# Performance work log

Hardware: AMD Instinct MI355X
Metric: run time of the kernel (lower is better)

The kernel has to match this reference:

```python
import jax, jax.numpy as jnp
import numpy as np

NUM_BLOCKS = 2
RES_LAYERS = 10
HID = 128
IN_CH = 256
MID_CH = 512
OUT_CH = 256
DILATIONS = [2 ** l for b in range(NUM_BLOCKS) for l in range(RES_LAYERS)]
GOOD = sum(DILATIONS)  # 2046
NLAYERS = NUM_BLOCKS * RES_LAYERS


def setup_inputs() -> dict:
    key = jax.random.key(0)
    ks = jax.random.split(key, 16)
    s = 0.05
    B, T = 8, 8192
    inp = {
        "inputs": jax.random.normal(ks[0], (B, IN_CH, T), dtype=jnp.float32),
        "Wi": jax.random.normal(ks[1], (HID, IN_CH), dtype=jnp.float32) * s,
        "bi": jax.random.normal(ks[2], (HID,), dtype=jnp.float32) * s,
        "Wf": jax.random.normal(ks[3], (NLAYERS, HID, HID, 2), dtype=jnp.float32) * s,
        "bf": jax.random.normal(ks[4], (NLAYERS, HID), dtype=jnp.float32) * s,
        "Wg": jax.random.normal(ks[5], (NLAYERS, HID, HID, 2), dtype=jnp.float32) * s,
        "bg": jax.random.normal(ks[6], (NLAYERS, HID), dtype=jnp.float32) * s,
        "Wr": jax.random.normal(ks[7], (NLAYERS, HID, HID), dtype=jnp.float32) * s,
        "br": jax.random.normal(ks[8], (NLAYERS, HID), dtype=jnp.float32) * s,
        "W1": jax.random.normal(ks[9], (MID_CH, HID), dtype=jnp.float32) * s,
        "b1": jax.random.normal(ks[10], (MID_CH,), dtype=jnp.float32) * s,
        "W2": jax.random.normal(ks[11], (OUT_CH, MID_CH), dtype=jnp.float32) * s,
        "b2": jax.random.normal(ks[12], (OUT_CH,), dtype=jnp.float32) * s,
    }
    return inp


def _dilated_k2(x, W, b, d):
    # x: [B, C, T] -> [B, C, T-d]
    y = jnp.einsum("oi,bit->bot", W[:, :, 0], x[:, :, :-d]) \
        + jnp.einsum("oi,bit->bot", W[:, :, 1], x[:, :, d:])
    return y + b[None, :, None]


def reference(inputs, Wi, bi, Wf, bf, Wg, bg, Wr, br, W1, b1, W2, b2):
    T = inputs.shape[2]
    target = T - GOOD
    res = jnp.einsum("oi,bit->bot", Wi, inputs) + bi[None, :, None]
    final = None
    for idx, d in enumerate(DILATIONS):
        f = jnp.tanh(_dilated_k2(res, Wf[idx], bf[idx], d))
        g = jax.nn.sigmoid(_dilated_k2(res, Wg[idx], bg[idx], d))
        out = f * g
        x = jnp.einsum("oi,bit->bot", Wr[idx], out) + br[idx][None, :, None]
        res = x + res[:, :, d:]
        # NOTE: original code computes split conv then immediately overwrites
        # it with x[:, :, -target:]; the split conv is dead code, so skip it.
        skip = x[:, :, -target:]
        final = skip if final is None else final + skip
    h = jax.nn.relu(final)
    h = jnp.einsum("oi,bit->bot", W1, h) + b1[None, :, None]
    h = jax.nn.relu(h)
    h = jnp.einsum("oi,bit->bot", W2, h) + b2[None, :, None]
    n, c, l = h.shape
    return jnp.transpose(h, (0, 2, 1)).reshape(n * l, c)
```

## Files before the change

kernel.cpp:

```cpp
#include <hip/hip_runtime.h>


#define TT 8192
#define HIDC 128
#define GOODC 2046
#define TGT 6146
#define NL 20
#define NTILES 1024
#define NBLK 512
#define GATE_CAP (1 << 18)
#define RDV_CAP (1 << 16)
#define STROWS 2046
#define STOFF(x) (((1 << ((x) % 10)) - 1) + 1023 * ((x) / 10))

typedef _Float16 half8_t __attribute__((ext_vector_type(8)));
typedef _Float16 half4_t __attribute__((ext_vector_type(4)));
typedef float floatx4 __attribute__((ext_vector_type(4)));

__device__ int g_progress[NTILES];
__device__ int g_qhead[8];
__device__ int g_arrive;
__device__ int g_broken;

__device__ __forceinline__ floatx4 mfma16(half8_t a, half8_t b, floatx4 c) {
  return __builtin_amdgcn_mfma_f32_16x16x32_f16(a, b, c, 0, 0, 0);
}
__device__ __forceinline__ float fast_sigmoid(float x) {
  return __builtin_amdgcn_rcpf(1.0f + __expf(-x));
}
__device__ __forceinline__ float fast_tanh(float x) {
  return 2.0f * __builtin_amdgcn_rcpf(1.0f + __expf(-2.0f * x)) - 1.0f;
}

__device__ __forceinline__ void cload4(const void* p0, const void* p1,
                                       const void* p2, const void* p3,
                                       floatx4& r0, floatx4& r1, floatx4& r2,
                                       floatx4& r3) {
  asm volatile(
      "global_load_dwordx4 %0, %4, off sc0\n\t"
      "global_load_dwordx4 %1, %5, off sc0\n\t"
      "global_load_dwordx4 %2, %6, off sc0\n\t"
      "global_load_dwordx4 %3, %7, off sc0\n\t"
      "s_waitcnt vmcnt(0)"
      : "=&v"(r0), "=&v"(r1), "=&v"(r2), "=&v"(r3)
      : "v"(p0), "v"(p1), "v"(p2), "v"(p3)
      : "memory");
}

__device__ __forceinline__ void spin_tile(int idx, int q) {
  int* f = &g_progress[idx];
  int it = 0;
  while (__hip_atomic_load(f, __ATOMIC_RELAXED, __HIP_MEMORY_SCOPE_AGENT) < q) {
    if (!(++it & 15) && __hip_atomic_load(&g_broken, __ATOMIC_RELAXED,
                                          __HIP_MEMORY_SCOPE_AGENT))
      break;
    if (it > GATE_CAP) {
      __hip_atomic_store(&g_broken, 1, __ATOMIC_RELAXED,
                         __HIP_MEMORY_SCOPE_AGENT);
      break;
    }
    __builtin_amdgcn_s_sleep(2);
  }
}

__global__ void prep_kernel(const float* __restrict__ Wi, const float* __restrict__ Wf,
                            const float* __restrict__ Wg, const float* __restrict__ Wr,
                            const float* __restrict__ W1, const float* __restrict__ W2,
                            _Float16* __restrict__ WIh, _Float16* __restrict__ WFG,
                            _Float16* __restrict__ WRh, _Float16* __restrict__ W1h,
                            _Float16* __restrict__ W2h) {
  int idx = blockIdx.x * blockDim.x + threadIdx.x;
  int stride = gridDim.x * blockDim.x;
  for (int i = idx; i < NTILES; i += stride) g_progress[i] = 0;
  for (int i = idx; i < 8; i += stride) g_qhead[i] = 0;
  if (idx == 0) { g_arrive = 0; g_broken = 0; }
  for (int i = idx; i < NL * 256 * 256; i += stride) {
    int l = i >> 16; int m = (i >> 8) & 255; int k = i & 255;
    int tap = k >> 7; int ci = k & 127;
    float v;
    if (m < 128) v = Wf[(((size_t)l * 128 + m) * 128 + ci) * 2 + tap];
    else         v = Wg[(((size_t)l * 128 + (m - 128)) * 128 + ci) * 2 + tap];
    WFG[i] = (_Float16)v;
  }
  for (int i = idx; i < NL * 128 * 128; i += stride) WRh[i] = (_Float16)Wr[i];
  for (int i = idx; i < 128 * 256; i += stride) WIh[i] = (_Float16)Wi[i];
  for (int i = idx; i < 512 * 128; i += stride) W1h[i] = (_Float16)W1[i];
  for (int i = idx; i < 256 * 512; i += stride) W2h[i] = (_Float16)W2[i];
}

__device__ __forceinline__ void phase_input(
    const float* __restrict__ ib, const _Float16* __restrict__ WIh,
    const float* __restrict__ bi, _Float16* __restrict__ pbout,
    _Float16* __restrict__ stout, int u0, int j, char* smem) {
  _Float16(*Rown)[136] = (_Float16(*)[136])smem;
  _Float16(*R0own)[136] = (_Float16(*)[136])(smem + 17408);
  _Float16(*Xs)[264] = (_Float16(*)[264])(smem + 17408);
  const int tid = threadIdx.x;
  const int lane = tid & 63;
  const int w = tid >> 6;
  const int ml = lane & 15;
  const int mq = lane >> 4;

#pragma unroll
  for (int it = 0; it < 4; ++it) {
    int i = it * 256 + tid;
    int n4 = i & 15;
    int kg = i >> 4;
    const float* src = ib + (size_t)(kg * 4) * TT + u0 + n4 * 4;
    floatx4 c0 = *(const floatx4*)(src);
    floatx4 c1 = *(const floatx4*)(src + TT);
    floatx4 c2 = *(const floatx4*)(src + 2 * TT);
    floatx4 c3 = *(const floatx4*)(src + 3 * TT);
#pragma unroll
    for (int tq = 0; tq < 4; ++tq) {
      half4_t h;
      h[0] = (_Float16)c0[tq]; h[1] = (_Float16)c1[tq];
      h[2] = (_Float16)c2[tq]; h[3] = (_Float16)c3[tq];
      *(half4_t*)&Xs[n4 * 4 + tq][kg * 4] = h;
    }
  }
  __syncthreads();

  floatx4 acc[2][4];
#pragma unroll
  for (int a = 0; a < 2; ++a)
#pragma unroll
    for (int c = 0; c < 4; ++c) acc[a][c] = floatx4{0.f, 0.f, 0.f, 0.f};
  const _Float16* Aw = WIh + (size_t)(32 * w + ml) * 256;
#pragma unroll
  for (int kk = 0; kk < 8; ++kk) {
    const int ko = kk * 32 + mq * 8;
    half8_t a0 = *(const half8_t*)(Aw + ko);
    half8_t a1 = *(const half8_t*)(Aw + 16 * 256 + ko);
#pragma unroll
    for (int nt = 0; nt < 4; ++nt) {
      half8_t bv = *(const half8_t*)&Xs[nt * 16 + ml][ko];
      acc[0][nt] = mfma16(a0, bv, acc[0][nt]);
      acc[1][nt] = mfma16(a1, bv, acc[1][nt]);
    }
  }
  __syncthreads();
  float* Xf = (float*)(smem + 17408);
#pragma unroll
  for (int mt = 0; mt < 2; ++mt) {
    const int mb = 32 * w + mt * 16 + mq * 4;
#pragma unroll
    for (int nt = 0; nt < 4; ++nt)
      *(floatx4*)&Xf[(nt * 16 + ml) * 132 + mb] = acc[mt][nt];
  }
  __syncthreads();
  half8_t hv[4];
#pragma unroll
  for (int it = 0; it < 4; ++it) {
    int i = it * 256 + tid;
    int n = i >> 4; int cq = i & 15;
    floatx4 x0 = *(const floatx4*)&Xf[n * 132 + cq * 8];
    floatx4 x1 = *(const floatx4*)&Xf[n * 132 + cq * 8 + 4];
    floatx4 b0 = *(const floatx4*)(bi + cq * 8);
    floatx4 b1v = *(const floatx4*)(bi + cq * 8 + 4);
#pragma unroll
    for (int tq = 0; tq < 4; ++tq) {
      hv[it][tq] = (_Float16)(x0[tq] + b0[tq]);
      hv[it][4 + tq] = (_Float16)(x1[tq] + b1v[tq]);
    }
  }
  __syncthreads();
#pragma unroll
  for (int it = 0; it < 4; ++it) {
    int i = it * 256 + tid;
    int n = i >> 4; int cq = i & 15;
    *(half8_t*)&Rown[n][cq * 8] = hv[it];
    *(half8_t*)&R0own[n][cq * 8] = hv[it];
    if (n == 63) {
      *(half8_t*)(pbout + (size_t)(u0 + 63) * HIDC + cq * 8) = hv[it];
      if (j == 63)
        *(half8_t*)(stout + cq * 8) = hv[it];
    }
  }
}

__device__ __forceinline__ void phase_layer(
    const _Float16* __restrict__ pbin, _Float16* __restrict__ pbout,
    const _Float16* __restrict__ stin, _Float16* __restrict__ stout,
    const _Float16* __restrict__ WFGl, const _Float16* __restrict__ WRl,
    const float* __restrict__ bfl, const float* __restrict__ bgl,
    const float* __restrict__ brl, int d, int u0, int ext, int nst,
    bool use_st, char* smem) {
  _Float16(*Rown)[136] = (_Float16(*)[136])smem;
  _Float16(*Xs0)[136] = (_Float16(*)[136])(smem + 34816);
  const int tid = threadIdx.x;
  const int lane = tid & 63;
  const int w = tid >> 6;
  const int ml = lane & 15;
  const int mq = lane >> 4;

  const int dd = d < 64 ? d : 64;
  const int nch = dd << 4;
  {
    const void* sp[4];
    floatx4 rr[4];
#pragma unroll
    for (int k = 0; k < 4; ++k) {
      int i = tid + (k << 8);
      int row = i >> 4, cc = i & 15;
      const _Float16* src;
      if (use_st) {
        src = stin + (size_t)(u0 - 4096 + row) * HIDC + cc * 8;
      } else {
        int p = u0 - d + row;
        if (p < 0) p = 0;
        src = pbin + (size_t)p * HIDC + cc * 8;
      }
      sp[k] = (i < nch) ? (const void*)src
                        : (use_st ? (const void*)stin : (const void*)pbin);
    }
    cload4(sp[0], sp[1], sp[2], sp[3], rr[0], rr[1], rr[2], rr[3]);
#pragma unroll
    for (int k = 0; k < 4; ++k) {
      int i = tid + (k << 8);
      if (i < nch) {
        int row = i >> 4, cc = i & 15;
        *(floatx4*)&Xs0[row][cc * 8] = rr[k];
      }
    }
  }
  __syncthreads();

  const _Float16* brow0[4];
  const _Float16* brow1[4];
#pragma unroll
  for (int nt = 0; nt < 4; ++nt) {
    int n = nt * 16 + ml;
    brow1[nt] = &Rown[n][0];
    brow0[nt] = (n < dd) ? &Xs0[n][0] : &Rown[n - d][0];
  }

  floatx4 accF[2][4], accG[2][4];
#pragma unroll
  for (int a = 0; a < 2; ++a)
#pragma unroll
    for (int cc = 0; cc < 4; ++cc) {
      accF[a][cc] = floatx4{0.f, 0.f, 0.f, 0.f};
      accG[a][cc] = floatx4{0.f, 0.f, 0.f, 0.f};
    }
  const _Float16* Af = WFGl + (size_t)(32 * w + ml) * 256;
  const _Float16* Ag = Af + 128 * 256;
#pragma unroll
  for (int h = 0; h < 2; ++h) {
#pragma unroll
    for (int kk = 0; kk < 4; ++kk) {
      const int ko = kk * 32 + mq * 8;
      const int kw = h * 128 + ko;
      half8_t aF0 = *(const half8_t*)(Af + kw);
      half8_t aF1 = *(const half8_t*)(Af + 16 * 256 + kw);
      half8_t aG0 = *(const half8_t*)(Ag + kw);
      half8_t aG1 = *(const half8_t*)(Ag + 16 * 256 + kw);
#pragma unroll
      for (int nt = 0; nt < 4; ++nt) {
        half8_t bv = *(const half8_t*)((h ? brow1[nt] : brow0[nt]) + ko);
        accF[0][nt] = mfma16(aF0, bv, accF[0][nt]);
        accF[1][nt] = mfma16(aF1, bv, accF[1][nt]);
        accG[0][nt] = mfma16(aG0, bv, accG[0][nt]);
        accG[1][nt] = mfma16(aG1, bv, accG[1][nt]);
      }
    }
  }

  half4_t og[2][4];
#pragma unroll
  for (int mt = 0; mt < 2; ++mt) {
    const int mb = 32 * w + mt * 16 + mq * 4;
    floatx4 bfv = *(const floatx4*)(bfl + mb);
    floatx4 bgv = *(const floatx4*)(bgl + mb);
#pragma unroll
    for (int nt = 0; nt < 4; ++nt) {
#pragma unroll
      for (int r = 0; r < 4; ++r) {
        float fv = fast_tanh(accF[mt][nt][r] + bfv[r]);
        float gv = fast_sigmoid(accG[mt][nt][r] + bgv[r]);
        og[mt][nt][r] = (_Float16)(fv * gv);
      }
    }
  }
  __syncthreads();

  _Float16(*Os)[136] = Xs0;
#pragma unroll
  for (int mt = 0; mt < 2; ++mt) {
    const int mb = 32 * w + mt * 16 + mq * 4;
#pragma unroll
    for (int nt = 0; nt < 4; ++nt)
      *(half4_t*)&Os[nt * 16 + ml][mb] = og[mt][nt];
  }
  __syncthreads();

  floatx4 accX[2][4];
#pragma unroll
  for (int a = 0; a < 2; ++a)
#pragma unroll
    for (int cc = 0; cc < 4; ++cc) accX[a][cc] = floatx4{0.f, 0.f, 0.f, 0.f};
  const _Float16* Ar = WRl + (size_t)(32 * w + ml) * 128;
#pragma unroll
  for (int kk = 0; kk < 4; ++kk) {
    const int ko = kk * 32 + mq * 8;
    half8_t a0 = *(const half8_t*)(Ar + ko);
    half8_t a1 = *(const half8_t*)(Ar + 16 * 128 + ko);
#pragma unroll
    for (int nt = 0; nt < 4; ++nt) {
      half8_t bv = *(const half8_t*)&Os[nt * 16 + ml][ko];
      accX[0][nt] = mfma16(a0, bv, accX[0][nt]);
      accX[1][nt] = mfma16(a1, bv, accX[1][nt]);
    }
  }

  half4_t xo[2][4];
#pragma unroll
  for (int mt = 0; mt < 2; ++mt) {
    const int mb = 32 * w + mt * 16 + mq * 4;
    floatx4 brv = *(const floatx4*)(brl + mb);
#pragma unroll
    for (int nt = 0; nt < 4; ++nt) {
      const int n = nt * 16 + ml;
      half4_t rold = *(const half4_t*)&Rown[n][mb];
#pragma unroll
      for (int r = 0; r < 4; ++r)
        xo[mt][nt][r] = (_Float16)(accX[mt][nt][r] + brv[r] + (float)rold[r]);
    }
  }
  __syncthreads();

#pragma unroll
  for (int mt = 0; mt < 2; ++mt) {
    const int mb = 32 * w + mt * 16 + mq * 4;
#pragma unroll
    for (int nt = 0; nt < 4; ++nt)
      *(half4_t*)&Rown[nt * 16 + ml][mb] = xo[mt][nt];
  }
  __syncthreads();

  for (int i = tid; i < (ext << 4); i += 256) {
    int row = 64 - ext + (i >> 4);
    int cc = i & 15;
    half8_t v = *(const half8_t*)&Rown[row][cc * 8];
    int p = u0 + row;
    *(half8_t*)(pbout + (size_t)p * HIDC + cc * 8) = v;
    if (nst && p >= 4096 - nst)
      *(half8_t*)(stout + (size_t)(p - 4096 + nst) * HIDC + cc * 8) = v;
  }
}

__device__ __forceinline__ void phase_head(
    const _Float16* __restrict__ W1h, const _Float16* __restrict__ W2h,
    const float* __restrict__ b1, const float* __restrict__ b2,
    float* __restrict__ outb, int u0, char* smem) {
  _Float16(*Rown)[136] = (_Float16(*)[136])smem;
  _Float16(*R0own)[136] = (_Float16(*)[136])(smem + 17408);
  _Float16* Hs = (_Float16*)(smem + 34816);
  _Float16* H1s = (_Float16*)(smem + 17408);
  const int tid = threadIdx.x;
  const int lane = tid & 63;
  const int w = tid >> 6;
  const int ml = lane & 15;
  const int mq = lane >> 4;

#pragma unroll
  for (int it = 0; it < 4; ++it) {
    int i = it * 256 + tid;
    int n = i >> 4; int cq = i & 15;
    half8_t a = *(const half8_t*)&Rown[n][cq * 8];
    half8_t z = *(const half8_t*)&R0own[n][cq * 8];
    half8_t h;
#pragma unroll
    for (int tq = 0; tq < 8; ++tq) {
      float v = (float)a[tq] - (float)z[tq];
      h[tq] = (_Float16)(v > 0.f ? v : 0.f);
    }
    *(half8_t*)&Hs[n * 136 + cq * 8] = h;
  }
  __syncthreads();

  floatx4 accO[4][4];
#pragma unroll
  for (int a = 0; a < 4; ++a)
#pragma unroll
    for (int c = 0; c < 4; ++c) accO[a][c] = floatx4{0.f, 0.f, 0.f, 0.f};

  for (int p = 0; p < 4; ++p) {
    floatx4 acc1[2][4];
#pragma unroll
    for (int a = 0; a < 2; ++a)
#pragma unroll
      for (int c = 0; c < 4; ++c) acc1[a][c] = floatx4{0.f, 0.f, 0.f, 0.f};
    const _Float16* A1 = W1h + (size_t)(128 * p + 32 * w + ml) * 128;
#pragma unroll
    for (int kk = 0; kk < 4; ++kk) {
      const int ko = kk * 32 + mq * 8;
      half8_t av0 = *(const half8_t*)(A1 + ko);
      half8_t av1 = *(const half8_t*)(A1 + 16 * 128 + ko);
#pragma unroll
      for (int nt = 0; nt < 4; ++nt) {
        half8_t bv = *(const half8_t*)&Hs[(nt * 16 + ml) * 136 + ko];
        acc1[0][nt] = mfma16(av0, bv, acc1[0][nt]);
        acc1[1][nt] = mfma16(av1, bv, acc1[1][nt]);
      }
    }
    __syncthreads();
#pragma unroll
    for (int mt = 0; mt < 2; ++mt) {
      const int kc = 32 * w + mt * 16 + mq * 4;
      floatx4 bv = *(const floatx4*)(b1 + 128 * p + kc);
#pragma unroll
      for (int nt = 0; nt < 4; ++nt) {
        half4_t h;
#pragma unroll
        for (int r = 0; r < 4; ++r) {
          float v = acc1[mt][nt][r] + bv[r];
          h[r] = (_Float16)(v > 0.f ? v : 0.f);
        }
        *(half4_t*)&H1s[(nt * 16 + ml) * 136 + kc] = h;
      }
    }
    __syncthreads();
    const _Float16* A2 = W2h + (size_t)(64 * w + ml) * 512 + p * 128;
#pragma unroll
    for (int kk = 0; kk < 4; ++kk) {
      const int ko = kk * 32 + mq * 8;
#pragma unroll
      for (int nt = 0; nt < 4; ++nt) {
        half8_t bv = *(const half8_t*)&H1s[(nt * 16 + ml) * 136 + ko];
#pragma unroll
        for (int mt = 0; mt < 4; ++mt) {
          half8_t av = *(const half8_t*)(A2 + (size_t)(mt * 16) * 512 + ko);
          accO[mt][nt] = mfma16(av, bv, accO[mt][nt]);
        }
      }
    }
    __syncthreads();
  }

  _Float16* Ot = (_Float16*)(smem + 17408);
#pragma unroll
  for (int mt = 0; mt < 4; ++mt) {
    const int m = 64 * w + mt * 16 + mq * 4;
    floatx4 bv = *(const floatx4*)(b2 + m);
#pragma unroll
    for (int nt = 0; nt < 4; ++nt) {
      const int n = nt * 16 + ml;
      half4_t h;
#pragma unroll
      for (int r = 0; r < 4; ++r) h[r] = (_Float16)(accO[mt][nt][r] + bv[r]);
      *(half4_t*)&Ot[n * 264 + m] = h;
    }
  }
  __syncthreads();
#pragma unroll
  for (int it = 0; it < 8; ++it) {
    int i = it * 256 + tid;
    int n = i >> 5;
    int g = i & 31;
    int u = u0 + n;
    if (u >= GOODC) {
      half8_t v = *(const half8_t*)&Ot[n * 264 + g * 8];
      float* dst = outb + (size_t)(u - GOODC) * 256 + g * 8;
      floatx4 v0, v1;
#pragma unroll
      for (int tq = 0; tq < 4; ++tq) { v0[tq] = (float)v[tq]; v1[tq] = (float)v[4 + tq]; }
      *(floatx4*)dst = v0;
      *(floatx4*)(dst + 4) = v1;
    }
  }
}

__global__ __launch_bounds__(256, 2) void mega_kernel(
    const float* __restrict__ inp, const _Float16* __restrict__ WIh,
    const float* __restrict__ bi, const _Float16* __restrict__ WFG,
    const _Float16* __restrict__ WRh, const float* __restrict__ bf,
    const float* __restrict__ bg, const float* __restrict__ br,
    const _Float16* __restrict__ W1h, const _Float16* __restrict__ W2h,
    const float* __restrict__ b1, const float* __restrict__ b2,
    _Float16* __restrict__ ST, _Float16* __restrict__ Ph,
    _Float16* __restrict__ Qh, float* __restrict__ out) {
  __shared__ __align__(16) char smem[52224];
  __shared__ int s_slot, s_bb, s_light;
  const int tid = threadIdx.x;

  if (tid == 0) {
    unsigned xcd;
    asm volatile("s_getreg_b32 %0, hwreg(HW_REG_XCC_ID)" : "=s"(xcd));
    xcd &= 7;
    int slot = __hip_atomic_fetch_add(&g_qhead[xcd], 1, __ATOMIC_RELAXED,
                                      __HIP_MEMORY_SCOPE_AGENT);
    __hip_atomic_fetch_add(&g_arrive, 1, __ATOMIC_RELEASE,
                           __HIP_MEMORY_SCOPE_AGENT);
    int ok = 1, it = 0;
    while (__hip_atomic_load(&g_arrive, __ATOMIC_ACQUIRE,
                             __HIP_MEMORY_SCOPE_AGENT) < NBLK) {
      if (++it > RDV_CAP) {
        ok = 0;
        __hip_atomic_store(&g_broken, 1, __ATOMIC_RELAXED,
                           __HIP_MEMORY_SCOPE_AGENT);
        break;
      }
      __builtin_amdgcn_s_sleep(8);
    }
    int light = ok;
    if (ok) {
#pragma unroll
      for (int x = 0; x < 8; ++x)
        light &= (__hip_atomic_load(&g_qhead[x], __ATOMIC_RELAXED,
                                    __HIP_MEMORY_SCOPE_AGENT) == NBLK / 8);
    }
    if (light) { s_bb = (int)xcd; s_slot = slot; }
    else       { s_bb = blockIdx.x >> 6; s_slot = blockIdx.x & 63; }
    s_light = light;
  }
  __syncthreads();
  const int slot = s_slot;
  const int bb = s_bb;
  const int light = s_light;

  _Float16* STb = ST + (size_t)bb * STROWS * HIDC;
  _Float16* Phb = Ph + (size_t)bb * TT * HIDC;
  _Float16* Qhb = Qh + (size_t)bb * TT * HIDC;
  const float* ib = inp + (size_t)bb * 256 * TT;
  float* outb = out + (size_t)bb * TGT * 256;

#pragma unroll 1
  for (int tt = 0; tt < 2; ++tt) {
    const int j = slot + tt * 64;
    const int u0 = j * 64;
#pragma unroll 1
    for (int q = 0; q < 22; ++q) {
      if (q >= 1 && q <= 20) {
        const int dcur = 1 << ((q - 1) % 10);
        const int jraw = j - ((dcur + 63) >> 6);
        int jwar = -1;
        if (q >= 2) {
          const int dp = 1 << ((q - 2) % 10);
          int cand = j + ((dp + 63) >> 6);
          const int hi = (j & 64) ? 127 : 63;
          if (cand <= hi) jwar = cand;
        }
        if (tid == 0 && jraw >= 0) spin_tile(bb * 128 + jraw, q);
        if (tid == 1 && jwar >= 0) spin_tile(bb * 128 + jwar, q);
        __syncthreads();
        if (!light) __builtin_amdgcn_fence(__ATOMIC_ACQUIRE, "agent");
      }

      if (q == 0) {
        phase_input(ib, WIh, bi, Qhb, STb , u0, j, smem);
      } else if (q <= 20) {
        const int l = q - 1;
        const int d = 1 << (l % 10);
        const _Float16* pbin = ((q - 1) & 1) ? Phb : Qhb;
        _Float16* pbout = (q & 1) ? Phb : Qhb;
        const _Float16* stin = STb + (size_t)STOFF(q - 1) * HIDC;
        _Float16* stout = STb + (size_t)STOFF(q <= 19 ? q : 0) * HIDC;
        const int ext = (q <= 19) ? ((1 << (q % 10)) < 64 ? (1 << (q % 10)) : 64) : 0;
        const int nst = (j < 64 && q <= 19) ? (1 << (q % 10)) : 0;
        const bool use_st = (j >= 64) && (u0 - d < 4096);
        phase_layer(pbin, pbout, stin, stout, WFG + (size_t)l * 65536,
                    WRh + (size_t)l * 16384, bf + l * 128, bg + l * 128,
                    br + l * 128, d, u0, ext, nst, use_st, smem);
      } else if (j >= 31) {
        phase_head(W1h, W2h, b1, b2, outb, u0, smem);
      }

      if (q <= 20) {
        if (light) {
          asm volatile("s_waitcnt vmcnt(0)" ::: "memory");
        } else {
          __builtin_amdgcn_fence(__ATOMIC_RELEASE, "agent");
        }
        __syncthreads();
        if (tid == 0)
          __hip_atomic_store(&g_progress[bb * 128 + j], q + 1,
                             __ATOMIC_RELAXED, __HIP_MEMORY_SCOPE_AGENT);
      } else {
        __syncthreads();
      }
    }
  }
}

extern "C" void kernel_launch(void* const* d_in, const int* in_sizes, int n_in,
                              void* d_out, int out_size, void* d_ws, size_t ws_size,
                              hipStream_t stream) {
  const float* inputs = (const float*)d_in[0];
  const float* Wi = (const float*)d_in[1];
  const float* bi = (const float*)d_in[2];
  const float* Wf = (const float*)d_in[3];
  const float* bf = (const float*)d_in[4];
  const float* Wg = (const float*)d_in[5];
  const float* bg = (const float*)d_in[6];
  const float* Wr = (const float*)d_in[7];
  const float* br = (const float*)d_in[8];
  const float* W1 = (const float*)d_in[9];
  const float* b1 = (const float*)d_in[10];
  const float* W2 = (const float*)d_in[11];
  const float* b2 = (const float*)d_in[12];
  float* out = (float*)d_out;

  char* ws = (char*)d_ws;
  _Float16* ST  = (_Float16*)(ws + 0);
  _Float16* Ph  = (_Float16*)(ws + 16777216);
  _Float16* Qh  = (_Float16*)(ws + 33554432);
  _Float16* WFG = (_Float16*)(ws + 50331648);
  _Float16* WRh = (_Float16*)(ws + 52953088);
  _Float16* WIh = (_Float16*)(ws + 53608448);
  _Float16* W1h = (_Float16*)(ws + 53673984);
  _Float16* W2h = (_Float16*)(ws + 53805056);

  prep_kernel<<<dim3(512), dim3(256), 0, stream>>>(Wi, Wf, Wg, Wr, W1, W2,
                                                   WIh, WFG, WRh, W1h, W2h);
  mega_kernel<<<dim3(NBLK), dim3(256), 0, stream>>>(
      inputs, WIh, bi, WFG, WRh, bf, bg, br, W1h, W2h, b1, b2,
      ST, Ph, Qh, out);
}
```

Before: 904.7 us.

## Double time tile to 128 columns, one tile per block, drop staging buffer

Each block now owns a single 128-column time tile instead of two 64-column tiles processed sequentially. Each weight fragment loaded per layer is reused across twice as many columns, the separate ST staging path for the batch half-boundary is removed, and the input residual R0 is kept in global memory instead of shared memory. The cost is more accumulator registers per thread, larger shared memory (69KB, which may hurt the two-blocks-per-CU occupancy), and a serialized dependency chain with coarser granularity. Spin sleep is also shortened.

After: 834.7 us. 1.08x faster.

```diff
diff --git a/kernel.cpp b/kernel.cpp
--- a/kernel.cpp
+++ b/kernel.cpp
@@ -6,12 +6,12 @@
 #define GOODC 2046
 #define TGT 6146
 #define NL 20
-#define NTILES 1024
+#define TILE 128
+#define NTB 64
+#define NTILES 512
 #define NBLK 512
 #define GATE_CAP (1 << 18)
 #define RDV_CAP (1 << 16)
-#define STROWS 2046
-#define STOFF(x) (((1 << ((x) % 10)) - 1) + 1023 * ((x) / 10))
 
 typedef _Float16 half8_t __attribute__((ext_vector_type(8)));
 typedef _Float16 half4_t __attribute__((ext_vector_type(4)));
@@ -32,6 +32,27 @@
   return 2.0f * __builtin_amdgcn_rcpf(1.0f + __expf(-2.0f * x)) - 1.0f;
 }
 
+__device__ __forceinline__ void cload8(
+    const void* p0, const void* p1, const void* p2, const void* p3,
+    const void* p4, const void* p5, const void* p6, const void* p7,
+    floatx4& r0, floatx4& r1, floatx4& r2, floatx4& r3,
+    floatx4& r4, floatx4& r5, floatx4& r6, floatx4& r7) {
+  asm volatile(
+      "global_load_dwordx4 %0, %8, off sc0\n\t"
+      "global_load_dwordx4 %1, %9, off sc0\n\t"
+      "global_load_dwordx4 %2, %10, off sc0\n\t"
+      "global_load_dwordx4 %3, %11, off sc0\n\t"
+      "global_load_dwordx4 %4, %12, off sc0\n\t"
+      "global_load_dwordx4 %5, %13, off sc0\n\t"
+      "global_load_dwordx4 %6, %14, off sc0\n\t"
+      "global_load_dwordx4 %7, %15, off sc0\n\t"
+      "s_waitcnt vmcnt(0)"
+      : "=&v"(r0), "=&v"(r1), "=&v"(r2), "=&v"(r3),
+        "=&v"(r4), "=&v"(r5), "=&v"(r6), "=&v"(r7)
+      : "v"(p0), "v"(p1), "v"(p2), "v"(p3),
+        "v"(p4), "v"(p5), "v"(p6), "v"(p7)
+      : "memory");
+}
 __device__ __forceinline__ void cload4(const void* p0, const void* p1,
                                        const void* p2, const void* p3,
                                        floatx4& r0, floatx4& r1, floatx4& r2,
@@ -59,7 +80,7 @@
                          __HIP_MEMORY_SCOPE_AGENT);
       break;
     }
-    __builtin_amdgcn_s_sleep(2);
+    __builtin_amdgcn_s_sleep(1);
   }
 }
 
@@ -88,13 +109,13 @@
   for (int i = idx; i < 256 * 512; i += stride) W2h[i] = (_Float16)W2[i];
 }
 
-__device__ __forceinline__ void phase_input(
+__device__ __forceinline__ void input_half(
     const float* __restrict__ ib, const _Float16* __restrict__ WIh,
-    const float* __restrict__ bi, _Float16* __restrict__ pbout,
-    _Float16* __restrict__ stout, int u0, int j, char* smem) {
+    const float* __restrict__ bi, _Float16* __restrict__ R0g,
+    _Float16* __restrict__ pbout, int u0t, int h, char* smem) {
   _Float16(*Rown)[136] = (_Float16(*)[136])smem;
-  _Float16(*R0own)[136] = (_Float16(*)[136])(smem + 17408);
-  _Float16(*Xs)[264] = (_Float16(*)[264])(smem + 17408);
+  _Float16(*Xs)[264] = (_Float16(*)[264])(smem + 34816);
+  const int u0 = u0t + 64 * h;
   const int tid = threadIdx.x;
   const int lane = tid & 63;
   const int w = tid >> 6;
@@ -113,10 +134,10 @@
     floatx4 c3 = *(const floatx4*)(src + 3 * TT);
 #pragma unroll
     for (int tq = 0; tq < 4; ++tq) {
-      half4_t h;
-      h[0] = (_Float16)c0[tq]; h[1] = (_Float16)c1[tq];
-      h[2] = (_Float16)c2[tq]; h[3] = (_Float16)c3[tq];
-      *(half4_t*)&Xs[n4 * 4 + tq][kg * 4] = h;
+      half4_t hh;
+      hh[0] = (_Float16)c0[tq]; hh[1] = (_Float16)c1[tq];
+      hh[2] = (_Float16)c2[tq]; hh[3] = (_Float16)c3[tq];
+      *(half4_t*)&Xs[n4 * 4 + tq][kg * 4] = hh;
     }
   }
   __syncthreads();
@@ -140,7 +161,7 @@
     }
   }
   __syncthreads();
-  float* Xf = (float*)(smem + 17408);
+  float* Xf = (float*)(smem + 34816);
 #pragma unroll
   for (int mt = 0; mt < 2; ++mt) {
     const int mb = 32 * w + mt * 16 + mq * 4;
@@ -149,7 +170,6 @@
       *(floatx4*)&Xf[(nt * 16 + ml) * 132 + mb] = acc[mt][nt];
   }
   __syncthreads();
-  half8_t hv[4];
 #pragma unroll
   for (int it = 0; it < 4; ++it) {
     int i = it * 256 + tid;
@@ -158,34 +178,25 @@
     floatx4 x1 = *(const floatx4*)&Xf[n * 132 + cq * 8 + 4];
     floatx4 b0 = *(const floatx4*)(bi + cq * 8);
     floatx4 b1v = *(const floatx4*)(bi + cq * 8 + 4);
+    half8_t hh;
 #pragma unroll
     for (int tq = 0; tq < 4; ++tq) {
-      hv[it][tq] = (_Float16)(x0[tq] + b0[tq]);
-      hv[it][4 + tq] = (_Float16)(x1[tq] + b1v[tq]);
-    }
-  }
-  __syncthreads();
-#pragma unroll
-  for (int it = 0; it < 4; ++it) {
-    int i = it * 256 + tid;
-    int n = i >> 4; int cq = i & 15;
-    *(half8_t*)&Rown[n][cq * 8] = hv[it];
-    *(half8_t*)&R0own[n][cq * 8] = hv[it];
-    if (n == 63) {
-      *(half8_t*)(pbout + (size_t)(u0 + 63) * HIDC + cq * 8) = hv[it];
-      if (j == 63)
-        *(half8_t*)(stout + cq * 8) = hv[it];
-    }
-  }
+      hh[tq] = (_Float16)(x0[tq] + b0[tq]);
+      hh[4 + tq] = (_Float16)(x1[tq] + b1v[tq]);
+    }
+    *(half8_t*)&Rown[64 * h + n][cq * 8] = hh;
+    *(half8_t*)(R0g + (size_t)(u0 + n) * HIDC + cq * 8) = hh;
+    if (h == 1 && n == 63)
+      *(half8_t*)(pbout + (size_t)(u0 + n) * HIDC + cq * 8) = hh;
+  }
+  __syncthreads();
 }
 
 __device__ __forceinline__ void phase_layer(
     const _Float16* __restrict__ pbin, _Float16* __restrict__ pbout,
-    const _Float16* __restrict__ stin, _Float16* __restrict__ stout,
     const _Float16* __restrict__ WFGl, const _Float16* __restrict__ WRl,
     const float* __restrict__ bfl, const float* __restrict__ bgl,
-    const float* __restrict__ brl, int d, int u0, int ext, int nst,
-    bool use_st, char* smem) {
+    const float* __restrict__ brl, int d, int u0, int ext, char* smem) {
   _Float16(*Rown)[136] = (_Float16(*)[136])smem;
   _Float16(*Xs0)[136] = (_Float16(*)[136])(smem + 34816);
   const int tid = threadIdx.x;
@@ -194,52 +205,45 @@
   const int ml = lane & 15;
   const int mq = lane >> 4;
 
-  const int dd = d < 64 ? d : 64;
+  const int dd = d < TILE ? d : TILE;
   const int nch = dd << 4;
   {
-    const void* sp[4];
-    floatx4 rr[4];
-#pragma unroll
-    for (int k = 0; k < 4; ++k) {
+    const void* sp[8];
+#pragma unroll
+    for (int k = 0; k < 8; ++k) {
       int i = tid + (k << 8);
       int row = i >> 4, cc = i & 15;
-      const _Float16* src;
-      if (use_st) {
-        src = stin + (size_t)(u0 - 4096 + row) * HIDC + cc * 8;
-      } else {
-        int p = u0 - d + row;
-        if (p < 0) p = 0;
-        src = pbin + (size_t)p * HIDC + cc * 8;
-      }
-      sp[k] = (i < nch) ? (const void*)src
-                        : (use_st ? (const void*)stin : (const void*)pbin);
-    }
-    cload4(sp[0], sp[1], sp[2], sp[3], rr[0], rr[1], rr[2], rr[3]);
-#pragma unroll
-    for (int k = 0; k < 4; ++k) {
+      int p = u0 - d + row;
+      if (p < 0) p = 0;
+      sp[k] = (i < nch) ? (const void*)(pbin + (size_t)p * HIDC + cc * 8)
+                        : (const void*)pbin;
+    }
+    floatx4 rr0, rr1, rr2, rr3, rr4, rr5, rr6, rr7;
+    cload8(sp[0], sp[1], sp[2], sp[3], sp[4], sp[5], sp[6], sp[7],
+           rr0, rr1, rr2, rr3, rr4, rr5, rr6, rr7);
+    floatx4 rr[8] = {rr0, rr1, rr2, rr3, rr4, rr5, rr6, rr7};
+#pragma unroll
+    for (int k = 0; k < 8; ++k) {
       int i = tid + (k << 8);
-      if (i < nch) {
-        int row = i >> 4, cc = i & 15;
-        *(floatx4*)&Xs0[row][cc * 8] = rr[k];
-      }
-    }
-  }
-  __syncthreads();
-
-  const _Float16* brow0[4];
-  const _Float16* brow1[4];
-#pragma unroll
-  for (int nt = 0; nt < 4; ++nt) {
+      if (i < nch) *(floatx4*)&Xs0[i >> 4][(i & 15) * 8] = rr[k];
+    }
+  }
+  __syncthreads();
+
+  const _Float16* brow0[8];
+  const _Float16* brow1[8];
+#pragma unroll
+  for (int nt = 0; nt < 8; ++nt) {
     int n = nt * 16 + ml;
     brow1[nt] = &Rown[n][0];
     brow0[nt] = (n < dd) ? &Xs0[n][0] : &Rown[n - d][0];
   }
 
-  floatx4 accF[2][4], accG[2][4];
+  floatx4 accF[2][8], accG[2][8];
 #pragma unroll
   for (int a = 0; a < 2; ++a)
 #pragma unroll
-    for (int cc = 0; cc < 4; ++cc) {
+    for (int cc = 0; cc < 8; ++cc) {
       accF[a][cc] = floatx4{0.f, 0.f, 0.f, 0.f};
       accG[a][cc] = floatx4{0.f, 0.f, 0.f, 0.f};
     }
@@ -256,7 +260,7 @@
       half8_t aG0 = *(const half8_t*)(Ag + kw);
       half8_t aG1 = *(const half8_t*)(Ag + 16 * 256 + kw);
 #pragma unroll
-      for (int nt = 0; nt < 4; ++nt) {
+      for (int nt = 0; nt < 8; ++nt) {
         half8_t bv = *(const half8_t*)((h ? brow1[nt] : brow0[nt]) + ko);
         accF[0][nt] = mfma16(aF0, bv, accF[0][nt]);
         accF[1][nt] = mfma16(aF1, bv, accF[1][nt]);
@@ -266,14 +270,14 @@
     }
   }
 
-  half4_t og[2][4];
+  half4_t og[2][8];
 #pragma unroll
   for (int mt = 0; mt < 2; ++mt) {
     const int mb = 32 * w + mt * 16 + mq * 4;
     floatx4 bfv = *(const floatx4*)(bfl + mb);
     floatx4 bgv = *(const floatx4*)(bgl + mb);
 #pragma unroll
-    for (int nt = 0; nt < 4; ++nt) {
+    for (int nt = 0; nt < 8; ++nt) {
 #pragma unroll
       for (int r = 0; r < 4; ++r) {
         float fv = fast_tanh(accF[mt][nt][r] + bfv[r]);
@@ -289,16 +293,16 @@
   for (int mt = 0; mt < 2; ++mt) {
     const int mb = 32 * w + mt * 16 + mq * 4;
 #pragma unroll
-    for (int nt = 0; nt < 4; ++nt)
+    for (int nt = 0; nt < 8; ++nt)
       *(half4_t*)&Os[nt * 16 + ml][mb] = og[mt][nt];
   }
   __syncthreads();
 
-  floatx4 accX[2][4];
+  floatx4 accX[2][8];
 #pragma unroll
   for (int a = 0; a < 2; ++a)
 #pragma unroll
-    for (int cc = 0; cc < 4; ++cc) accX[a][cc] = floatx4{0.f, 0.f, 0.f, 0.f};
+    for (int cc = 0; cc < 8; ++cc) accX[a][cc] = floatx4{0.f, 0.f, 0.f, 0.f};
   const _Float16* Ar = WRl + (size_t)(32 * w + ml) * 128;
 #pragma unroll
   for (int kk = 0; kk < 4; ++kk) {
@@ -306,20 +310,20 @@
     half8_t a0 = *(const half8_t*)(Ar + ko);
     half8_t a1 = *(const half8_t*)(Ar + 16 * 128 + ko);
 #pragma unroll
-    for (int nt = 0; nt < 4; ++nt) {
+    for (int nt = 0; nt < 8; ++nt) {
       half8_t bv = *(const half8_t*)&Os[nt * 16 + ml][ko];
       accX[0][nt] = mfma16(a0, bv, accX[0][nt]);
       accX[1][nt] = mfma16(a1, bv, accX[1][nt]);
     }
   }
 
-  half4_t xo[2][4];
+  half4_t xo[2][8];
 #pragma unroll
   for (int mt = 0; mt < 2; ++mt) {
     const int mb = 32 * w + mt * 16 + mq * 4;
     floatx4 brv = *(const floatx4*)(brl + mb);
 #pragma unroll
-    for (int nt = 0; nt < 4; ++nt) {
+    for (int nt = 0; nt < 8; ++nt) {
       const int n = nt * 16 + ml;
       half4_t rold = *(const half4_t*)&Rown[n][mb];
 #pragma unroll
@@ -333,49 +337,58 @@
   for (int mt = 0; mt < 2; ++mt) {
     const int mb = 32 * w + mt * 16 + mq * 4;
 #pragma unroll
-    for (int nt = 0; nt < 4; ++nt)
+    for (int nt = 0; nt < 8; ++nt)
       *(half4_t*)&Rown[nt * 16 + ml][mb] = xo[mt][nt];
   }
   __syncthreads();
 
   for (int i = tid; i < (ext << 4); i += 256) {
-    int row = 64 - ext + (i >> 4);
+    int row = TILE - ext + (i >> 4);
     int cc = i & 15;
-    half8_t v = *(const half8_t*)&Rown[row][cc * 8];
-    int p = u0 + row;
-    *(half8_t*)(pbout + (size_t)p * HIDC + cc * 8) = v;
-    if (nst && p >= 4096 - nst)
-      *(half8_t*)(stout + (size_t)(p - 4096 + nst) * HIDC + cc * 8) = v;
-  }
-}
-
-__device__ __forceinline__ void phase_head(
-    const _Float16* __restrict__ W1h, const _Float16* __restrict__ W2h,
-    const float* __restrict__ b1, const float* __restrict__ b2,
-    float* __restrict__ outb, int u0, char* smem) {
+    *(half8_t*)(pbout + (size_t)(u0 + row) * HIDC + cc * 8) =
+        *(const half8_t*)&Rown[row][cc * 8];
+  }
+}
+
+__device__ __forceinline__ void head_half(
+    const _Float16* __restrict__ R0g, const _Float16* __restrict__ W1h,
+    const _Float16* __restrict__ W2h, const float* __restrict__ b1,
+    const float* __restrict__ b2, float* __restrict__ outb, int u0t, int h,
+    char* smem) {
   _Float16(*Rown)[136] = (_Float16(*)[136])smem;
-  _Float16(*R0own)[136] = (_Float16(*)[136])(smem + 17408);
   _Float16* Hs = (_Float16*)(smem + 34816);
-  _Float16* H1s = (_Float16*)(smem + 17408);
+  _Float16* H1s = (_Float16*)(smem + 34816 + 17408);
+  const int u0 = u0t + 64 * h;
   const int tid = threadIdx.x;
   const int lane = tid & 63;
   const int w = tid >> 6;
   const int ml = lane & 15;
   const int mq = lane >> 4;
 
-#pragma unroll
-  for (int it = 0; it < 4; ++it) {
-    int i = it * 256 + tid;
-    int n = i >> 4; int cq = i & 15;
-    half8_t a = *(const half8_t*)&Rown[n][cq * 8];
-    half8_t z = *(const half8_t*)&R0own[n][cq * 8];
-    half8_t h;
-#pragma unroll
-    for (int tq = 0; tq < 8; ++tq) {
-      float v = (float)a[tq] - (float)z[tq];
-      h[tq] = (_Float16)(v > 0.f ? v : 0.f);
-    }
-    *(half8_t*)&Hs[n * 136 + cq * 8] = h;
+  {
+    const void* sp[4];
+#pragma unroll
+    for (int it = 0; it < 4; ++it) {
+      int i = it * 256 + tid;
+      sp[it] = R0g + (size_t)(u0 + (i >> 4)) * HIDC + (i & 15) * 8;
+    }
+    floatx4 z0, z1, z2, z3;
+    cload4(sp[0], sp[1], sp[2], sp[3], z0, z1, z2, z3);
+    floatx4 zz[4] = {z0, z1, z2, z3};
+#pragma unroll
+    for (int it = 0; it < 4; ++it) {
+      int i = it * 256 + tid;
+      int n = i >> 4; int cq = i & 15;
+      half8_t a = *(const half8_t*)&Rown[64 * h + n][cq * 8];
+      half8_t zv = *(half8_t*)&zz[it];
+      half8_t hh;
+#pragma unroll
+      for (int tq = 0; tq < 8; ++tq) {
+        float v = (float)a[tq] - (float)zv[tq];
+        hh[tq] = (_Float16)(v > 0.f ? v : 0.f);
+      }
+      *(half8_t*)&Hs[n * 136 + cq * 8] = hh;
+    }
   }
   __syncthreads();
 
@@ -411,13 +424,13 @@
       floatx4 bv = *(const floatx4*)(b1 + 128 * p + kc);
 #pragma unroll
       for (int nt = 0; nt < 4; ++nt) {
-        half4_t h;
+        half4_t hh;
 #pragma unroll
         for (int r = 0; r < 4; ++r) {
           float v = acc1[mt][nt][r] + bv[r];
-          h[r] = (_Float16)(v > 0.f ? v : 0.f);
+          hh[r] = (_Float16)(v > 0.f ? v : 0.f);
         }
-        *(half4_t*)&H1s[(nt * 16 + ml) * 136 + kc] = h;
+        *(half4_t*)&H1s[(nt * 16 + ml) * 136 + kc] = hh;
       }
     }
     __syncthreads();
@@ -438,7 +451,7 @@
     __syncthreads();
   }
 
-  _Float16* Ot = (_Float16*)(smem + 17408);
+  _Float16* Ot = (_Float16*)(smem + 34816);
 #pragma unroll
   for (int mt = 0; mt < 4; ++mt) {
     const int m = 64 * w + mt * 16 + mq * 4;
@@ -446,10 +459,10 @@
 #pragma unroll
     for (int nt = 0; nt < 4; ++nt) {
       const int n = nt * 16 + ml;
-      half4_t h;
-#pragma unroll
-      for (int r = 0; r < 4; ++r) h[r] = (_Float16)(accO[mt][nt][r] + bv[r]);
-      *(half4_t*)&Ot[n * 264 + m] = h;
+      half4_t hh;
+#pragma unroll
+      for (int r = 0; r < 4; ++r) hh[r] = (_Float16)(accO[mt][nt][r] + bv[r]);
+      *(half4_t*)&Ot[n * 264 + m] = hh;
     }
   }
   __syncthreads();
@@ -469,6 +482,7 @@
       *(floatx4*)(dst + 4) = v1;
     }
   }
+  __syncthreads();
 }
 
 __global__ __launch_bounds__(256, 2) void mega_kernel(
@@ -478,10 +492,10 @@
     const float* __restrict__ bg, const float* __restrict__ br,
     const _Float16* __restrict__ W1h, const _Float16* __restrict__ W2h,
     const float* __restrict__ b1, const float* __restrict__ b2,
-    _Float16* __restrict__ ST, _Float16* __restrict__ Ph,
+    _Float16* __restrict__ R0g, _Float16* __restrict__ Ph,
     _Float16* __restrict__ Qh, float* __restrict__ out) {
-  __shared__ __align__(16) char smem[52224];
-  __shared__ int s_slot, s_bb, s_light;
+  __shared__ __align__(16) char smem[69632];
+  __shared__ int s_j, s_bb, s_light;
   const int tid = threadIdx.x;
 
   if (tid == 0) {
@@ -510,75 +524,74 @@
         light &= (__hip_atomic_load(&g_qhead[x], __ATOMIC_RELAXED,
                                     __HIP_MEMORY_SCOPE_AGENT) == NBLK / 8);
     }
-    if (light) { s_bb = (int)xcd; s_slot = slot; }
-    else       { s_bb = blockIdx.x >> 6; s_slot = blockIdx.x & 63; }
+    if (light) { s_bb = (int)xcd; s_j = slot; }
+    else       { s_bb = blockIdx.x >> 6; s_j = blockIdx.x & 63; }
     s_light = light;
   }
   __syncthreads();
-  const int slot = s_slot;
+  const int j = s_j;
   const int bb = s_bb;
   const int light = s_light;
-
-  _Float16* STb = ST + (size_t)bb * STROWS * HIDC;
+  const int u0 = j * TILE;
+
+  _Float16* R0b = R0g + (size_t)bb * TT * HIDC;
   _Float16* Phb = Ph + (size_t)bb * TT * HIDC;
   _Float16* Qhb = Qh + (size_t)bb * TT * HIDC;
   const float* ib = inp + (size_t)bb * 256 * TT;
   float* outb = out + (size_t)bb * TGT * 256;
+  int* myflag = &g_progress[bb * NTB + j];
 
 #pragma unroll 1
-  for (int tt = 0; tt < 2; ++tt) {
-    const int j = slot + tt * 64;
-    const int u0 = j * 64;
-#pragma unroll 1
-    for (int q = 0; q < 22; ++q) {
-      if (q >= 1 && q <= 20) {
-        const int dcur = 1 << ((q - 1) % 10);
-        const int jraw = j - ((dcur + 63) >> 6);
-        int jwar = -1;
-        if (q >= 2) {
-          const int dp = 1 << ((q - 2) % 10);
-          int cand = j + ((dp + 63) >> 6);
-          const int hi = (j & 64) ? 127 : 63;
-          if (cand <= hi) jwar = cand;
-        }
-        if (tid == 0 && jraw >= 0) spin_tile(bb * 128 + jraw, q);
-        if (tid == 1 && jwar >= 0) spin_tile(bb * 128 + jwar, q);
-        __syncthreads();
-        if (!light) __builtin_amdgcn_fence(__ATOMIC_ACQUIRE, "agent");
-      }
-
-      if (q == 0) {
-        phase_input(ib, WIh, bi, Qhb, STb , u0, j, smem);
-      } else if (q <= 20) {
-        const int l = q - 1;
-        const int d = 1 << (l % 10);
-        const _Float16* pbin = ((q - 1) & 1) ? Phb : Qhb;
-        _Float16* pbout = (q & 1) ? Phb : Qhb;
-        const _Float16* stin = STb + (size_t)STOFF(q - 1) * HIDC;
-        _Float16* stout = STb + (size_t)STOFF(q <= 19 ? q : 0) * HIDC;
-        const int ext = (q <= 19) ? ((1 << (q % 10)) < 64 ? (1 << (q % 10)) : 64) : 0;
-        const int nst = (j < 64 && q <= 19) ? (1 << (q % 10)) : 0;
-        const bool use_st = (j >= 64) && (u0 - d < 4096);
-        phase_layer(pbin, pbout, stin, stout, WFG + (size_t)l * 65536,
-                    WRh + (size_t)l * 16384, bf + l * 128, bg + l * 128,
-                    br + l * 128, d, u0, ext, nst, use_st, smem);
-      } else if (j >= 31) {
-        phase_head(W1h, W2h, b1, b2, outb, u0, smem);
-      }
-
-      if (q <= 20) {
-        if (light) {
-          asm volatile("s_waitcnt vmcnt(0)" ::: "memory");
-        } else {
-          __builtin_amdgcn_fence(__ATOMIC_RELEASE, "agent");
-        }
-        __syncthreads();
-        if (tid == 0)
-          __hip_atomic_store(&g_progress[bb * 128 + j], q + 1,
-                             __ATOMIC_RELAXED, __HIP_MEMORY_SCOPE_AGENT);
+  for (int q = 0; q < 22; ++q) {
+    if (q >= 1 && q <= 20) {
+      const int dcur = 1 << ((q - 1) % 10);
+      const int jraw = j - ((dcur + TILE - 1) >> 7);
+      int jwar = -1;
+      if (q >= 2) {
+        const int dp = 1 << ((q - 2) % 10);
+        int cand = j + ((dp + TILE - 1) >> 7);
+        if (cand <= NTB - 1) jwar = cand;
+      }
+      if (tid == 0 && jraw >= 0) spin_tile(bb * NTB + jraw, q);
+      if (tid == 1 && jwar >= 0) spin_tile(bb * NTB + jwar, q);
+      __syncthreads();
+      if (!light) __builtin_amdgcn_fence(__ATOMIC_ACQUIRE, "agent");
+    }
+
+    if (q == 0) {
+      input_half(ib, WIh, bi, R0b, Qhb, u0, 0, smem);
+      input_half(ib, WIh, bi, R0b, Qhb, u0, 1, smem);
+    } else if (q <= 20) {
+      const int l = q - 1;
+      const int d = 1 << (l % 10);
+      const _Float16* pbin = ((q - 1) & 1) ? Phb : Qhb;
+      _Float16* pbout = (q & 1) ? Phb : Qhb;
+      int ext = 0;
+      if (q <= 19) {
+        ext = 1 << (q % 10);
+        if (ext > TILE) ext = TILE;
+      }
+      phase_layer(pbin, pbout, WFG + (size_t)l * 65536,
+                  WRh + (size_t)l * 16384, bf + l * 128, bg + l * 128,
+                  br + l * 128, d, u0, ext, smem);
+    } else {
+      if (u0 + 127 >= GOODC) {
+        if (u0 + 63 >= GOODC)
+          head_half(R0b, W1h, W2h, b1, b2, outb, u0, 0, smem);
+        head_half(R0b, W1h, W2h, b1, b2, outb, u0, 1, smem);
+      }
+    }
+
+    if (q <= 20) {
+      if (light) {
+        asm volatile("s_waitcnt vmcnt(0)" ::: "memory");
       } else {
-        __syncthreads();
-      }
+        __builtin_amdgcn_fence(__ATOMIC_RELEASE, "agent");
+      }
+      __syncthreads();
+      if (tid == 0)
+        __hip_atomic_store(myflag, q + 1, __ATOMIC_RELAXED,
+                           __HIP_MEMORY_SCOPE_AGENT);
     }
   }
 }
@@ -602,7 +615,7 @@
   float* out = (float*)d_out;
 
   char* ws = (char*)d_ws;
-  _Float16* ST  = (_Float16*)(ws + 0);
+  _Float16* R0g = (_Float16*)(ws + 0);
   _Float16* Ph  = (_Float16*)(ws + 16777216);
   _Float16* Qh  = (_Float16*)(ws + 33554432);
   _Float16* WFG = (_Float16*)(ws + 50331648);
@@ -615,5 +628,5 @@
                                                    WIh, WFG, WRh, W1h, W2h);
   mega_kernel<<<dim3(NBLK), dim3(256), 0, stream>>>(
       inputs, WIh, bi, WFG, WRh, bf, bg, br, W1h, W2h, b1, b2,
-      ST, Ph, Qh, out);
-}
+      R0g, Ph, Qh, out);
+}
```
